# Kernel tuning notes

Hardware: AMD Instinct MI355X
Metric: run time of the kernel (lower is better)

The kernel has to match this reference:

```python
import jax, jax.numpy as jnp
import numpy as np

B, T, C = 2, 2048, 2048
H, HD = 16, 128          # n_head, head_dim
LORA = C // 4            # kv_lora_rank = n_embd // compression_ratio
RD = HD // 2             # qk_rope_dim
ND = HD - RD             # qk_nope_dim
THETA = 100000.0


def setup_inputs() -> dict:
    key = jax.random.key(0)
    k0, k1, k2, k3, k4 = jax.random.split(key, 5)
    s = 0.02
    return {
        "x": jax.random.normal(k0, (B, T, C), dtype=jnp.float32),
        "Wq": jax.random.normal(k1, (C, H * HD), dtype=jnp.float32) * s,
        "Wkva": jax.random.normal(k2, (C, LORA + RD), dtype=jnp.float32) * s,
        "Wkvb": jax.random.normal(k3, (LORA, H * ND), dtype=jnp.float32) * s,
        "Wo": jax.random.normal(k4, (H * HD, C), dtype=jnp.float32) * s,
    }


def apply_rope(x, theta=THETA):
    # x: [B, H, T, D] with D even; interleaved complex rotation (torch.view_as_complex style)
    b, h, t, d = x.shape
    freqs = 1.0 / (theta ** (jnp.arange(0, d, 2, dtype=jnp.float32) / d))  # [D/2]
    ang = jnp.arange(t, dtype=jnp.float32)[:, None] * freqs[None, :]       # [T, D/2]
    cos, sin = jnp.cos(ang), jnp.sin(ang)
    xr = x.reshape(b, h, t, d // 2, 2)
    x0, x1 = xr[..., 0], xr[..., 1]
    o0 = x0 * cos - x1 * sin
    o1 = x0 * sin + x1 * cos
    return jnp.stack([o0, o1], axis=-1).reshape(b, h, t, d)


def reference(x, Wq, Wkva, Wkvb, Wo):
    Bx, Tx, Cx = x.shape
    # query projection -> [B, H, T, HD]
    q = (x @ Wq).reshape(Bx, Tx, H, HD).transpose(0, 2, 1, 3)
    # compressed KV + shared (MQA) rope key
    ckv = x @ Wkva                                  # [B, T, LORA+RD]
    kv_latent = ckv[..., :LORA]                     # [B, T, LORA]
    k_rope = ckv[..., LORA:]                        # [B, T, RD]
    # decompress nope part of K (== nope part of V)
    kv = (kv_latent @ Wkvb).reshape(Bx, Tx, H, ND).transpose(0, 2, 1, 3)  # [B,H,T,ND]
    k_rope = jnp.broadcast_to(k_rope[:, None, :, :], (Bx, H, Tx, RD))
    q_nope, q_rope = q[..., :ND], q[..., ND:]
    q_rope = apply_rope(q_rope)
    k_rope = apply_rope(k_rope)
    qf = jnp.concatenate([q_nope, q_rope], axis=-1)               # [B,H,T,HD]
    kf = jnp.concatenate([kv, k_rope], axis=-1)                   # [B,H,T,HD]
    vf = jnp.concatenate([kv, jnp.zeros_like(k_rope)], axis=-1)   # [B,H,T,HD]
    scale = 1.0 / np.sqrt(HD).astype(np.float32)
    att = jnp.einsum("bhtd,bhsd->bhts", qf, kf) * scale           # [B,H,T,T]
    causal = jnp.tril(jnp.ones((Tx, Tx), dtype=bool))
    att = jnp.where(causal, att, -jnp.inf)
    att = jax.nn.softmax(att, axis=-1)
    y = jnp.einsum("bhts,bhsd->bhtd", att, vf)                    # [B,H,T,HD]
    y = y.transpose(0, 2, 1, 3).reshape(Bx, Tx, H * HD)
    return y @ Wo
```

## Files before the change

kernel.cpp:

```cpp
#include <hip/hip_runtime.h>
#include <hip/hip_bf16.h>
#include <math.h>

#define B_ 2
#define T_ 2048
#define C_ 2048
#define H_ 16
#define HD_ 128
#define LORA_ 512
#define RD_ 64
#define ND_ 64
#define BT_ (B_*T_)
#define NKVA_ 576
#define NKVAP_ 640
#define LOG2_THETA 16.609640474436812f

typedef __bf16 bf16x8 __attribute__((ext_vector_type(8)));
typedef float  f32x4  __attribute__((ext_vector_type(4)));

#define MFMA16(a,b,c) __builtin_amdgcn_mfma_f32_16x16x32_bf16((a),(b),(c),0,0,0)

__device__ static inline void load_lds16(const __bf16* g, __bf16* l) {
  auto* lp = (__attribute__((address_space(3))) char*)(uintptr_t)(l);
  auto* gp = (const __attribute__((address_space(1))) char*)(g);
  __builtin_amdgcn_global_load_lds(gp, lp, 16, 0, 0);
}

__device__ static inline unsigned pkbf(float a, float b) {
  union { __bf16 h[2]; unsigned u; } v;
  v.h[0] = (__bf16)a; v.h[1] = (__bf16)b;
  return v.u;
}

__global__ __launch_bounds__(256) void k_cast_x(const float* __restrict__ x,
                                                __bf16* __restrict__ xb, int n) {
  int idx = blockIdx.x * 256 + threadIdx.x;
  if (idx < n) xb[idx] = (__bf16)x[idx];
}

__global__ __launch_bounds__(256) void k_tcast(const float* __restrict__ src,
                                               __bf16* __restrict__ dst,
                                               int K, int N, int NP) {
  __shared__ float tile[32][33];
  int k0 = blockIdx.x * 32;
  int n0 = blockIdx.y * 32;
  int tx = threadIdx.x & 31, ty = threadIdx.x >> 5;
  for (int i = ty; i < 32; i += 8) {
    int n = n0 + tx;
    tile[i][tx] = (n < N) ? src[(size_t)(k0 + i) * N + n] : 0.0f;
  }
  __syncthreads();
  for (int i = ty; i < 32; i += 8) {
    dst[(size_t)(n0 + i) * K + k0 + tx] = (__bf16)tile[tx][i];
  }
}

__global__ __launch_bounds__(256) void k_tcast_wo(const float* __restrict__ Wo,
                                                  __bf16* __restrict__ dst) {
  __shared__ float tile[32][33];
  int kc0 = blockIdx.x * 32;
  int n0  = blockIdx.y * 32;
  int rbase = (kc0 >> 6) * 128 + (kc0 & 63);
  int tx = threadIdx.x & 31, ty = threadIdx.x >> 5;
  for (int i = ty; i < 32; i += 8)
    tile[i][tx] = Wo[(size_t)(rbase + i) * C_ + n0 + tx];
  __syncthreads();
  for (int i = ty; i < 32; i += 8)
    dst[(size_t)(n0 + i) * 1024 + kc0 + tx] = (__bf16)tile[tx][i];
}

__global__ __launch_bounds__(256) void k_gemm_bt(const __bf16* __restrict__ A,
                                                 const __bf16* __restrict__ B,
                                                 float* __restrict__ C,
                                                 int M, int N, int K) {
  __shared__ __align__(16) __bf16 As[2][128 * 32];
  __shared__ __align__(16) __bf16 Bs[2][128 * 32];
  const int tid  = threadIdx.x;
  const int lane = tid & 63;
  const int wave = tid >> 6;
  const int bm = blockIdx.x, bn = blockIdx.y;
  const int r0 = tid >> 2;
  const int c8 = (tid & 3) * 8;
  const __bf16* Ag = A + (size_t)(bm * 128 + r0) * K + c8;
  const __bf16* Bg = B + (size_t)(bn * 128 + r0) * K + c8;
  const int wr = (wave >> 1) * 64, wc = (wave & 1) * 64;
  const int fr = lane & 15, fk = (lane >> 4) * 8;
  const f32x4 fzero = {0.f, 0.f, 0.f, 0.f};
  f32x4 acc[4][4];
#pragma unroll
  for (int i = 0; i < 4; ++i)
#pragma unroll
    for (int j = 0; j < 4; ++j) acc[i][j] = fzero;

  load_lds16(Ag,                  &As[0][tid * 8]);
  load_lds16(Ag + (size_t)64 * K, &As[0][tid * 8 + 2048]);
  load_lds16(Bg,                  &Bs[0][tid * 8]);
  load_lds16(Bg + (size_t)64 * K, &Bs[0][tid * 8 + 2048]);

  int buf = 0;
  for (int k0 = 0; k0 < K; k0 += 32) {
    __syncthreads();
    if (k0 + 32 < K) {
      const int nb = buf ^ 1;
      load_lds16(Ag + k0 + 32,                  &As[nb][tid * 8]);
      load_lds16(Ag + (size_t)64 * K + k0 + 32, &As[nb][tid * 8 + 2048]);
      load_lds16(Bg + k0 + 32,                  &Bs[nb][tid * 8]);
      load_lds16(Bg + (size_t)64 * K + k0 + 32, &Bs[nb][tid * 8 + 2048]);
    }
    bf16x8 af[4], bfg[4];
#pragma unroll
    for (int i = 0; i < 4; ++i) af[i]  = *(const bf16x8*)&As[buf][(wr + i * 16 + fr) * 32 + fk];
#pragma unroll
    for (int j = 0; j < 4; ++j) bfg[j] = *(const bf16x8*)&Bs[buf][(wc + j * 16 + fr) * 32 + fk];
#pragma unroll
    for (int i = 0; i < 4; ++i)
#pragma unroll
      for (int j = 0; j < 4; ++j)
        acc[i][j] = MFMA16(af[i], bfg[j], acc[i][j]);
    buf ^= 1;
  }
  const int rbase = (lane >> 4) * 4;
  float* Cb = C + (size_t)(bm * 128 + wr + rbase) * N + bn * 128 + wc + fr;
#pragma unroll
  for (int i = 0; i < 4; ++i)
#pragma unroll
    for (int j = 0; j < 4; ++j)
#pragma unroll
      for (int r = 0; r < 4; ++r)
        Cb[(size_t)(i * 16 + r) * N + j * 16] = acc[i][j][r];
}

__global__ __launch_bounds__(256) void k_rope_q(const float* __restrict__ q,
                                                __bf16* __restrict__ qf) {
  const float scale2 = 1.4426950408889634f / 11.313708498984760f;
  int idx = blockIdx.x * 256 + threadIdx.x;
  int d  = idx & 127;
  int t  = (idx >> 7) & 2047;
  int bh = idx >> 18;
  int h  = bh & 15, b = bh >> 4;
  const float* qrow = q + ((size_t)(b * T_ + t)) * 2048 + h * 128;
  float v;
  if (d < 64) {
    v = qrow[d];
  } else {
    int i = (d - 64) >> 1;
    float freq = exp2f(-((float)(2 * i) / 64.0f) * LOG2_THETA);
    float ang = (float)t * freq;
    float c = cosf(ang), s = sinf(ang);
    float x0 = qrow[64 + 2 * i], x1 = qrow[64 + 2 * i + 1];
    v = (d & 1) ? (x0 * s + x1 * c) : (x0 * c - x1 * s);
  }
  qf[idx] = (__bf16)(v * scale2);
}


__global__ __launch_bounds__(256) void k_rope_kf(const float* __restrict__ ckv,
                                                 __bf16* __restrict__ Kp) {
  int idx = blockIdx.x * 256 + threadIdx.x;
  int i = idx & 31;
  int t = (idx >> 5) & 2047;
  int h = (idx >> 16) & 15;
  int b = idx >> 20;
  const float* src = ckv + ((size_t)(b * T_ + t)) * NKVAP_ + 512;
  float freq = exp2f(-((float)(2 * i) / 64.0f) * LOG2_THETA);
  float ang = (float)t * freq;
  float c = cosf(ang), s = sinf(ang);
  float x0 = src[2 * i], x1 = src[2 * i + 1];
  float v0 = x0 * c - x1 * s;
  float v1 = x0 * s + x1 * c;
  int bh = b * 16 + h;
  int tile = t >> 6, cg = (t >> 4) & 3, frk = t & 15;
  int kg = 2 + (i >> 4), qd = (i >> 2) & 3, e = (2 * i) & 7;
  size_t off = (((size_t)(bh * 32 + tile) * 16) + cg * 4 + kg) * 512
             + (qd * 16 + frk) * 8 + e;
  *(unsigned*)(Kp + off) = pkbf(v0, v1);
}

__global__ __launch_bounds__(256) void k_cast_kvl(const float* __restrict__ ckv,
                                                  __bf16* __restrict__ kvl) {
  int idx = blockIdx.x * 256 + threadIdx.x;
  int r = idx >> 9, c = idx & 511;
  kvl[idx] = (__bf16)ckv[(size_t)r * NKVAP_ + c];
}

__global__ __launch_bounds__(256) void k_pack_kv(const float* __restrict__ kv,
                                                 __bf16* __restrict__ Kp,
                                                 __bf16* __restrict__ Vp) {
  __shared__ float tile[64][65];
  const int bh = blockIdx.x;
  const int b = bh >> 4, h = bh & 15;
  const int t0 = blockIdx.y * 64;
  const int tilei = t0 >> 6;
  const int tid = threadIdx.x;
  const int i0 = tid >> 4, d4 = (tid & 15) * 4;
  const int kg = d4 >> 5, qd = (d4 >> 3) & 3, e = d4 & 7;
#pragma unroll
  for (int p = 0; p < 4; ++p) {
    int i = i0 + p * 16;
    const float* src = kv + ((size_t)(b * T_ + t0 + i)) * 1024 + h * 64 + d4;
    float4 v = *(const float4*)src;
    tile[i][d4] = v.x; tile[i][d4 + 1] = v.y; tile[i][d4 + 2] = v.z; tile[i][d4 + 3] = v.w;
    union { __bf16 hh[4]; uint2 u; } o;
    o.hh[0] = (__bf16)v.x; o.hh[1] = (__bf16)v.y; o.hh[2] = (__bf16)v.z; o.hh[3] = (__bf16)v.w;
    const int cg = i >> 4, frk = i & 15;
    size_t koff = (((size_t)(bh * 32 + tilei) * 16) + cg * 4 + kg) * 512
                + (qd * 16 + frk) * 8 + e;
    *(uint2*)(Kp + koff) = o.u;
  }
  __syncthreads();
  const int dd = tid >> 2, tc0 = (tid & 3) * 16;
  __bf16 outv[16];
#pragma unroll
  for (int j = 0; j < 16; ++j) outv[j] = (__bf16)tile[tc0 + j][dd];
  const int g = dd >> 4, frv = dd & 15;
  const int ks = tc0 >> 5, qv = (tc0 >> 3) & 3;
  size_t voff = (((size_t)(bh * 32 + tilei) * 8) + g * 2 + ks) * 512
              + (qv * 16 + frv) * 8;
  *(bf16x8*)(Vp + voff) = *(bf16x8*)&outv[0];
  *(bf16x8*)(Vp + voff + 128) = *(bf16x8*)&outv[8];
}

__global__ __launch_bounds__(512, 4) void k_attn(const __bf16* __restrict__ qf,
                                                 const __bf16* __restrict__ Kp,
                                                 const __bf16* __restrict__ Vp,
                                                 __bf16* __restrict__ yc) {
  const int blk = blockIdx.x;
  const int bh = blk & 31;
  const int qt = 31 - (blk >> 5);
  const int b = bh >> 4, h = bh & 15;
  const int qbase = qt * 64;
  const int tid = threadIdx.x;
  const int lane = tid & 63, wave = tid >> 6;
  const int w4 = wave & 3, par = wave >> 2;
  const int fr = lane & 15, quad = lane >> 4, fk8 = quad * 8;

  __shared__ __align__(16) f32x4 mrgO[4][64][4];
  __shared__ float mrgML[4][64][2];

  const int qi = qbase + w4 * 16 + fr;
  const __bf16* qb = qf + ((size_t)bh * T_ + qi) * HD_;
  bf16x8 aq[4];
#pragma unroll
  for (int g = 0; g < 4; ++g) aq[g] = *(const bf16x8*)(qb + g * 32 + fk8);

  const f32x4 fzero = {0.f, 0.f, 0.f, 0.f};
  f32x4 accO[4];
#pragma unroll
  for (int g = 0; g < 4; ++g) accO[g] = fzero;
  float m = -1e30f, l = 0.f;

  const __bf16* kb = Kp + (size_t)bh * 32 * 8192 + (size_t)lane * 8;
  const __bf16* vb = Vp + (size_t)bh * 32 * 4096 + (size_t)lane * 8;
  const int srcA = (quad & 1) * 32 + fr, srcB = srcA + 16;
  const int hi = quad >> 1;

  for (int s0 = par * 64; s0 <= qbase; s0 += 128) {
    const __bf16* kt = kb + (size_t)(s0 >> 6) * 8192;
    const __bf16* vt = vb + (size_t)(s0 >> 6) * 4096;

    bf16x8 kr[4][4];
#pragma unroll
    for (int cg = 0; cg < 4; ++cg)
#pragma unroll
      for (int kg = 0; kg < 4; ++kg)
        kr[cg][kg] = *(const bf16x8*)(kt + (cg * 4 + kg) * 512);

    f32x4 accST[4];
#pragma unroll
    for (int cg = 0; cg < 4; ++cg) accST[cg] = fzero;
    __builtin_amdgcn_s_setprio(1);
#pragma unroll
    for (int cg = 0; cg < 4; ++cg) {
#pragma unroll
      for (int kg = 0; kg < 4; ++kg)
        accST[cg] = MFMA16(kr[cg][kg], aq[kg], accST[cg]);
    }
    __builtin_amdgcn_s_setprio(0);

    bf16x8 vr[4][2];
#pragma unroll
    for (int g = 0; g < 4; ++g)
#pragma unroll
      for (int ks = 0; ks < 2; ++ks)
        vr[g][ks] = *(const bf16x8*)(vt + (g * 2 + ks) * 512);

    float lmax = -1e30f;
    if (s0 == qbase) {
#pragma unroll
      for (int cg = 0; cg < 4; ++cg) {
#pragma unroll
        for (int r = 0; r < 4; ++r) {
          const int key = s0 + cg * 16 + quad * 4 + r;
          float v = accST[cg][r];
          v = (key <= qi) ? v : -1e30f;
          accST[cg][r] = v;
          lmax = fmaxf(lmax, v);
        }
      }
    } else {
#pragma unroll
      for (int cg = 0; cg < 4; ++cg) {
#pragma unroll
        for (int r = 0; r < 4; ++r) lmax = fmaxf(lmax, accST[cg][r]);
      }
    }
    lmax = fmaxf(lmax, __shfl_xor(lmax, 16, 64));
    lmax = fmaxf(lmax, __shfl_xor(lmax, 32, 64));

    if (!__all(lmax <= m + 8.0f)) {
      const float mn = fmaxf(m, lmax);
      const float alpha = exp2f(m - mn);
      l *= alpha;
#pragma unroll
      for (int g = 0; g < 4; ++g)
#pragma unroll
        for (int r = 0; r < 4; ++r) accO[g][r] *= alpha;
      m = mn;
    }

    float lsum = 0.f;
    unsigned pk0[4], pk1[4];
#pragma unroll
    for (int cg = 0; cg < 4; ++cg) {
      float p0 = exp2f(accST[cg][0] - m);
      float p1 = exp2f(accST[cg][1] - m);
      float p2 = exp2f(accST[cg][2] - m);
      float p3 = exp2f(accST[cg][3] - m);
      lsum += (p0 + p1) + (p2 + p3);
      pk0[cg] = pkbf(p0, p1);
      pk1[cg] = pkbf(p2, p3);
    }
    lsum += __shfl_xor(lsum, 16, 64);
    lsum += __shfl_xor(lsum, 32, 64);
    l += lsum;

#pragma unroll
    for (int ks = 0; ks < 2; ++ks) {
      int a0 = __shfl((int)pk0[2 * ks], srcA, 64);
      int b0 = __shfl((int)pk0[2 * ks + 1], srcA, 64);
      int a1 = __shfl((int)pk1[2 * ks], srcA, 64);
      int b1 = __shfl((int)pk1[2 * ks + 1], srcA, 64);
      int a2 = __shfl((int)pk0[2 * ks], srcB, 64);
      int b2 = __shfl((int)pk0[2 * ks + 1], srcB, 64);
      int a3 = __shfl((int)pk1[2 * ks], srcB, 64);
      int b3 = __shfl((int)pk1[2 * ks + 1], srcB, 64);
      union { int i[4]; bf16x8 v; } pf;
      pf.i[0] = hi ? b0 : a0;
      pf.i[1] = hi ? b1 : a1;
      pf.i[2] = hi ? b2 : a2;
      pf.i[3] = hi ? b3 : a3;
      __builtin_amdgcn_s_setprio(1);
#pragma unroll
      for (int g = 0; g < 4; ++g)
        accO[g] = MFMA16(vr[g][ks], pf.v, accO[g]);
      __builtin_amdgcn_s_setprio(0);
    }
  }

  if (par) {
#pragma unroll
    for (int g = 0; g < 4; ++g) mrgO[w4][lane][g] = accO[g];
    mrgML[w4][lane][0] = m;
    mrgML[w4][lane][1] = l;
  }
  __syncthreads();
  if (!par) {
    const float m1 = mrgML[w4][lane][0];
    const float l1 = mrgML[w4][lane][1];
    const float mn = fmaxf(m, m1);
    const float a0 = exp2f(m - mn), a1 = exp2f(m1 - mn);
    const float lt = l * a0 + l1 * a1;
    const float linv = 1.0f / lt;
    __bf16* yb = yc + ((size_t)(b * T_ + qi)) * 1024 + h * 64 + quad * 4;
#pragma unroll
    for (int g = 0; g < 4; ++g) {
      f32x4 o1 = mrgO[w4][lane][g];
      union { unsigned u[2]; uint2 v; } o;
      o.u[0] = pkbf((accO[g][0] * a0 + o1[0] * a1) * linv,
                    (accO[g][1] * a0 + o1[1] * a1) * linv);
      o.u[1] = pkbf((accO[g][2] * a0 + o1[2] * a1) * linv,
                    (accO[g][3] * a0 + o1[3] * a1) * linv);
      *(uint2*)(yb + g * 16) = o.v;
    }
  }
}

extern "C" void kernel_launch(void* const* d_in, const int* in_sizes, int n_in,
                              void* d_out, int out_size, void* d_ws, size_t ws_size,
                              hipStream_t stream) {
  const float* x    = (const float*)d_in[0];
  const float* Wq   = (const float*)d_in[1];
  const float* Wkva = (const float*)d_in[2];
  const float* Wkvb = (const float*)d_in[3];
  const float* Wo   = (const float*)d_in[4];
  float* out = (float*)d_out;
  char* ws = (char*)d_ws;

  size_t off = 0;
  __bf16* xb    = (__bf16*)(ws + off); off += (size_t)BT_ * C_ * 2;
  __bf16* WqT   = (__bf16*)(ws + off); off += (size_t)2048 * 2048 * 2;
  __bf16* WkvaT = (__bf16*)(ws + off); off += (size_t)NKVAP_ * 2048 * 2;
  __bf16* WkvbT = (__bf16*)(ws + off); off += (size_t)1024 * 512 * 2;
  __bf16* WoTc  = (__bf16*)(ws + off); off += (size_t)2048 * 1024 * 2;
  float*  q     = (float*)(ws + off);  off += (size_t)BT_ * 2048 * 4;
  float*  ckv   = (float*)(ws + off);  off += (size_t)BT_ * NKVAP_ * 4;
  __bf16* kvl   = (__bf16*)(ws + off); off += (size_t)BT_ * 512 * 2;
  float*  kv    = (float*)(ws + off);  off += (size_t)BT_ * 1024 * 4;
  __bf16* qfb   = (__bf16*)(ws + off); off += (size_t)B_ * H_ * T_ * HD_ * 2;
  __bf16* yc    = (__bf16*)(ws + off); off += (size_t)BT_ * 1024 * 2;
  __bf16* Kp = (__bf16*)q;
  __bf16* Vp = (__bf16*)((char*)q + (size_t)B_ * H_ * T_ * HD_ * 2);

  k_cast_x<<<(BT_ * C_) / 256, 256, 0, stream>>>(x, xb, BT_ * C_);
  k_tcast<<<dim3(2048 / 32, 2048 / 32), 256, 0, stream>>>(Wq, WqT, 2048, 2048, 2048);
  k_tcast<<<dim3(2048 / 32, NKVAP_ / 32), 256, 0, stream>>>(Wkva, WkvaT, 2048, NKVA_, NKVAP_);
  k_tcast<<<dim3(512 / 32, 1024 / 32), 256, 0, stream>>>(Wkvb, WkvbT, 512, 1024, 1024);
  k_tcast_wo<<<dim3(1024 / 32, 2048 / 32), 256, 0, stream>>>(Wo, WoTc);

  k_gemm_bt<<<dim3(BT_ / 128, 2048 / 128), 256, 0, stream>>>(xb, WqT, q, BT_, 2048, 2048);
  k_gemm_bt<<<dim3(BT_ / 128, NKVAP_ / 128), 256, 0, stream>>>(xb, WkvaT, ckv, BT_, NKVAP_, 2048);

  k_rope_q<<<(B_ * H_ * T_ * HD_) / 256, 256, 0, stream>>>(q, qfb);
  k_cast_kvl<<<(BT_ * 512) / 256, 256, 0, stream>>>(ckv, kvl);

  k_gemm_bt<<<dim3(BT_ / 128, 1024 / 128), 256, 0, stream>>>(kvl, WkvbT, kv, BT_, 1024, 512);
  k_pack_kv<<<dim3(B_ * H_, T_ / 64), 256, 0, stream>>>(kv, Kp, Vp);
  k_rope_kf<<<(B_ * H_ * T_ * 32) / 256, 256, 0, stream>>>(ckv, Kp);

  k_attn<<<(T_ / 64) * B_ * H_, 512, 0, stream>>>(qfb, Kp, Vp, yc);

  k_gemm_bt<<<dim3(BT_ / 128, 2048 / 128), 256, 0, stream>>>(yc, WoTc, out, BT_, 2048, 1024);
}
```

Measured before the change: 336.1 us.

## Fuse Q and KV-A projections into one GEMM with rope and cast epilogues

The separate Q and compressed-KV GEMMs become a single launch over a combined weight matrix of 2688 rows, assuming WkvaT sits directly after WqT in the workspace. The epilogue applies scaling and RoPE and writes bf16 q straight into the attention layout. It writes the latent part of KV as bf16 and keeps only the rope columns of ckv in fp32. This removes the fp32 q round trip through memory plus the standalone rope_q and cast_kvl kernels. The cost is a heavier epilogue with per-element cos/sin evaluation and lane shuffles.

```diff
diff --git a/kernel.cpp b/kernel.cpp
--- a/kernel.cpp
+++ b/kernel.cpp
@@ -130,27 +130,121 @@
         Cb[(size_t)(i * 16 + r) * N + j * 16] = acc[i][j][r];
 }
 
-__global__ __launch_bounds__(256) void k_rope_q(const float* __restrict__ q,
-                                                __bf16* __restrict__ qf) {
+__global__ __launch_bounds__(256) void k_gemm_qkva(const __bf16* __restrict__ A,
+                                                   const __bf16* __restrict__ Bq,
+                                                   __bf16* __restrict__ qf,
+                                                   __bf16* __restrict__ kvl,
+                                                   float* __restrict__ ckv) {
+  const int K = 2048;
+  __shared__ __align__(16) __bf16 As[2][128 * 32];
+  __shared__ __align__(16) __bf16 Bs[2][128 * 32];
+  const int tid  = threadIdx.x;
+  const int lane = tid & 63;
+  const int wave = tid >> 6;
+  const int bm = blockIdx.x, bn = blockIdx.y;
+  const int r0 = tid >> 2;
+  const int c8 = (tid & 3) * 8;
+  const __bf16* Ag = A  + (size_t)(bm * 128 + r0) * K + c8;
+  const __bf16* Bg = Bq + (size_t)(bn * 128 + r0) * K + c8;
+  const int wr = (wave >> 1) * 64, wc = (wave & 1) * 64;
+  const int fr = lane & 15, fk = (lane >> 4) * 8;
+  const f32x4 fzero = {0.f, 0.f, 0.f, 0.f};
+  f32x4 acc[4][4];
+#pragma unroll
+  for (int i = 0; i < 4; ++i)
+#pragma unroll
+    for (int j = 0; j < 4; ++j) acc[i][j] = fzero;
+
+  load_lds16(Ag,                  &As[0][tid * 8]);
+  load_lds16(Ag + (size_t)64 * K, &As[0][tid * 8 + 2048]);
+  load_lds16(Bg,                  &Bs[0][tid * 8]);
+  load_lds16(Bg + (size_t)64 * K, &Bs[0][tid * 8 + 2048]);
+
+  int buf = 0;
+  for (int k0 = 0; k0 < K; k0 += 32) {
+    __syncthreads();
+    if (k0 + 32 < K) {
+      const int nb = buf ^ 1;
+      load_lds16(Ag + k0 + 32,                  &As[nb][tid * 8]);
+      load_lds16(Ag + (size_t)64 * K + k0 + 32, &As[nb][tid * 8 + 2048]);
+      load_lds16(Bg + k0 + 32,                  &Bs[nb][tid * 8]);
+      load_lds16(Bg + (size_t)64 * K + k0 + 32, &Bs[nb][tid * 8 + 2048]);
+    }
+    bf16x8 af[4], bfg[4];
+#pragma unroll
+    for (int i = 0; i < 4; ++i) af[i]  = *(const bf16x8*)&As[buf][(wr + i * 16 + fr) * 32 + fk];
+#pragma unroll
+    for (int j = 0; j < 4; ++j) bfg[j] = *(const bf16x8*)&Bs[buf][(wc + j * 16 + fr) * 32 + fk];
+#pragma unroll
+    for (int i = 0; i < 4; ++i)
+#pragma unroll
+      for (int j = 0; j < 4; ++j)
+        acc[i][j] = MFMA16(af[i], bfg[j], acc[i][j]);
+    buf ^= 1;
+  }
+
+  const int rbase = (lane >> 4) * 4;
   const float scale2 = 1.4426950408889634f / 11.313708498984760f;
-  int idx = blockIdx.x * 256 + threadIdx.x;
-  int d  = idx & 127;
-  int t  = (idx >> 7) & 2047;
-  int bh = idx >> 18;
-  int h  = bh & 15, b = bh >> 4;
-  const float* qrow = q + ((size_t)(b * T_ + t)) * 2048 + h * 128;
-  float v;
-  if (d < 64) {
-    v = qrow[d];
+
+  if (bn < 16) {
+    const int h = bn;
+#pragma unroll
+    for (int i = 0; i < 4; ++i) {
+#pragma unroll
+      for (int j = 0; j < 4; ++j) {
+        const int d = wc + j * 16 + fr;
+#pragma unroll
+        for (int r = 0; r < 4; ++r) {
+          const int tg = bm * 128 + wr + rbase + i * 16 + r;
+          const int b = tg >> 11, tin = tg & 2047;
+          float v = acc[i][j][r];
+          float vo = __shfl_xor(v, 1);
+          float o;
+          if (d < 64) {
+            o = v * scale2;
+          } else {
+            const int ip = (d - 64) >> 1;
+            float freq = exp2f(-((float)(2 * ip) / 64.0f) * LOG2_THETA);
+            float ang = (float)tin * freq;
+            float c = cosf(ang), s = sinf(ang);
+            o = ((fr & 1) == 0) ? (v * c - vo * s) : (vo * s + v * c);
+            o *= scale2;
+          }
+          float op = __shfl_xor(o, 1);
+          if ((fr & 1) == 0) {
+            *(unsigned*)(qf + (((size_t)(b * 16 + h) * 2048 + tin) * 128 + d)) =
+                pkbf(o, op);
+          }
+        }
+      }
+    }
+  } else if (bn < 20) {
+    const int cb = (bn - 16) * 128;
+#pragma unroll
+    for (int i = 0; i < 4; ++i) {
+#pragma unroll
+      for (int j = 0; j < 4; ++j) {
+        const int c = cb + wc + j * 16 + fr;
+#pragma unroll
+        for (int r = 0; r < 4; ++r) {
+          const int tg = bm * 128 + wr + rbase + i * 16 + r;
+          float v = acc[i][j][r];
+          float vo = __shfl_xor(v, 1);
+          if ((fr & 1) == 0)
+            *(unsigned*)(kvl + ((size_t)tg * 512 + c)) = pkbf(v, vo);
+        }
+      }
+    }
   } else {
-    int i = (d - 64) >> 1;
-    float freq = exp2f(-((float)(2 * i) / 64.0f) * LOG2_THETA);
-    float ang = (float)t * freq;
-    float c = cosf(ang), s = sinf(ang);
-    float x0 = qrow[64 + 2 * i], x1 = qrow[64 + 2 * i + 1];
-    v = (d & 1) ? (x0 * s + x1 * c) : (x0 * c - x1 * s);
-  }
-  qf[idx] = (__bf16)(v * scale2);
+    float* Cb = ckv + (size_t)(bm * 128 + wr + rbase) * NKVAP_ + 512 + wc + fr;
+#pragma unroll
+    for (int i = 0; i < 4; ++i)
+#pragma unroll
+      for (int j = 0; j < 4; ++j)
+#pragma unroll
+        for (int r = 0; r < 4; ++r)
+          Cb[(size_t)(i * 16 + r) * NKVAP_ + j * 16] = acc[i][j][r];
+  }
 }
 
 
@@ -176,13 +270,6 @@
   *(unsigned*)(Kp + off) = pkbf(v0, v1);
 }
 
-__global__ __launch_bounds__(256) void k_cast_kvl(const float* __restrict__ ckv,
-                                                  __bf16* __restrict__ kvl) {
-  int idx = blockIdx.x * 256 + threadIdx.x;
-  int r = idx >> 9, c = idx & 511;
-  kvl[idx] = (__bf16)ckv[(size_t)r * NKVAP_ + c];
-}
-
 __global__ __launch_bounds__(256) void k_pack_kv(const float* __restrict__ kv,
                                                  __bf16* __restrict__ Kp,
                                                  __bf16* __restrict__ Vp) {
@@ -417,11 +504,7 @@
   k_tcast<<<dim3(512 / 32, 1024 / 32), 256, 0, stream>>>(Wkvb, WkvbT, 512, 1024, 1024);
   k_tcast_wo<<<dim3(1024 / 32, 2048 / 32), 256, 0, stream>>>(Wo, WoTc);
 
-  k_gemm_bt<<<dim3(BT_ / 128, 2048 / 128), 256, 0, stream>>>(xb, WqT, q, BT_, 2048, 2048);
-  k_gemm_bt<<<dim3(BT_ / 128, NKVAP_ / 128), 256, 0, stream>>>(xb, WkvaT, ckv, BT_, NKVAP_, 2048);
-
-  k_rope_q<<<(B_ * H_ * T_ * HD_) / 256, 256, 0, stream>>>(q, qfb);
-  k_cast_kvl<<<(BT_ * 512) / 256, 256, 0, stream>>>(ckv, kvl);
+  k_gemm_qkva<<<dim3(BT_ / 128, 2688 / 128), 256, 0, stream>>>(xb, WqT, qfb, kvl, ckv);
 
   k_gemm_bt<<<dim3(BT_ / 128, 1024 / 128), 256, 0, stream>>>(kvl, WkvbT, kv, BT_, 1024, 512);
   k_pack_kv<<<dim3(B_ * H_, T_ / 64), 256, 0, stream>>>(kv, Kp, Vp);
```

Result: slower. 348.7 us (+3.7%).

## Split GEMM K dimension across two intra-block warp groups with LDS reduction

Applied to the files above, without the earlier changes.

Each GEMM block now runs 512 threads as two 256-thread halves. Each half accumulates the same 128x128 output tile over half of the K range, using its own double-buffered LDS region. At the end, one half writes its partial sums to LDS and the other adds them and stores to global memory. This doubles the waves per tile to hide latency, at the cost of 64KB LDS per block, an extra reduction pass and more register pressure under launch_bounds(512,4).

```diff
diff --git a/kernel.cpp b/kernel.cpp
--- a/kernel.cpp
+++ b/kernel.cpp
@@ -69,21 +69,25 @@
     dst[(size_t)(n0 + i) * 1024 + kc0 + tx] = (__bf16)tile[tx][i];
 }
 
-__global__ __launch_bounds__(256) void k_gemm_bt(const __bf16* __restrict__ A,
-                                                 const __bf16* __restrict__ B,
-                                                 float* __restrict__ C,
-                                                 int M, int N, int K) {
-  __shared__ __align__(16) __bf16 As[2][128 * 32];
-  __shared__ __align__(16) __bf16 Bs[2][128 * 32];
+__global__ __launch_bounds__(512, 4) void k_gemm_bt(const __bf16* __restrict__ A,
+                                                    const __bf16* __restrict__ B,
+                                                    float* __restrict__ C,
+                                                    int M, int N, int K) {
+  __shared__ __align__(16) char smem[65536];
   const int tid  = threadIdx.x;
+  const int half = tid >> 8;
+  const int tid_h = tid & 255;
   const int lane = tid & 63;
-  const int wave = tid >> 6;
+  const int wave4 = (tid >> 6) & 3;
   const int bm = blockIdx.x, bn = blockIdx.y;
-  const int r0 = tid >> 2;
-  const int c8 = (tid & 3) * 8;
-  const __bf16* Ag = A + (size_t)(bm * 128 + r0) * K + c8;
-  const __bf16* Bg = B + (size_t)(bn * 128 + r0) * K + c8;
-  const int wr = (wave >> 1) * 64, wc = (wave & 1) * 64;
+  const int Kh = K >> 1, kbase = half * Kh;
+  __bf16* As = (__bf16*)smem + (size_t)half * 16384;
+  __bf16* Bs = As + 8192;
+  const int r0 = tid_h >> 2;
+  const int c8 = (tid_h & 3) * 8;
+  const __bf16* Ag = A + (size_t)(bm * 128 + r0) * K + kbase + c8;
+  const __bf16* Bg = B + (size_t)(bn * 128 + r0) * K + kbase + c8;
+  const int wr = (wave4 >> 1) * 64, wc = (wave4 & 1) * 64;
   const int fr = lane & 15, fk = (lane >> 4) * 8;
   const f32x4 fzero = {0.f, 0.f, 0.f, 0.f};
   f32x4 acc[4][4];
@@ -92,26 +96,28 @@
 #pragma unroll
     for (int j = 0; j < 4; ++j) acc[i][j] = fzero;
 
-  load_lds16(Ag,                  &As[0][tid * 8]);
-  load_lds16(Ag + (size_t)64 * K, &As[0][tid * 8 + 2048]);
-  load_lds16(Bg,                  &Bs[0][tid * 8]);
-  load_lds16(Bg + (size_t)64 * K, &Bs[0][tid * 8 + 2048]);
+  load_lds16(Ag,                  &As[tid_h * 8]);
+  load_lds16(Ag + (size_t)64 * K, &As[tid_h * 8 + 2048]);
+  load_lds16(Bg,                  &Bs[tid_h * 8]);
+  load_lds16(Bg + (size_t)64 * K, &Bs[tid_h * 8 + 2048]);
 
   int buf = 0;
-  for (int k0 = 0; k0 < K; k0 += 32) {
+  for (int k0 = 0; k0 < Kh; k0 += 32) {
     __syncthreads();
-    if (k0 + 32 < K) {
+    if (k0 + 32 < Kh) {
       const int nb = buf ^ 1;
-      load_lds16(Ag + k0 + 32,                  &As[nb][tid * 8]);
-      load_lds16(Ag + (size_t)64 * K + k0 + 32, &As[nb][tid * 8 + 2048]);
-      load_lds16(Bg + k0 + 32,                  &Bs[nb][tid * 8]);
-      load_lds16(Bg + (size_t)64 * K + k0 + 32, &Bs[nb][tid * 8 + 2048]);
+      load_lds16(Ag + k0 + 32,                  &As[nb * 4096 + tid_h * 8]);
+      load_lds16(Ag + (size_t)64 * K + k0 + 32, &As[nb * 4096 + tid_h * 8 + 2048]);
+      load_lds16(Bg + k0 + 32,                  &Bs[nb * 4096 + tid_h * 8]);
+      load_lds16(Bg + (size_t)64 * K + k0 + 32, &Bs[nb * 4096 + tid_h * 8 + 2048]);
     }
     bf16x8 af[4], bfg[4];
 #pragma unroll
-    for (int i = 0; i < 4; ++i) af[i]  = *(const bf16x8*)&As[buf][(wr + i * 16 + fr) * 32 + fk];
-#pragma unroll
-    for (int j = 0; j < 4; ++j) bfg[j] = *(const bf16x8*)&Bs[buf][(wc + j * 16 + fr) * 32 + fk];
+    for (int i = 0; i < 4; ++i)
+      af[i]  = *(const bf16x8*)&As[buf * 4096 + (wr + i * 16 + fr) * 32 + fk];
+#pragma unroll
+    for (int j = 0; j < 4; ++j)
+      bfg[j] = *(const bf16x8*)&Bs[buf * 4096 + (wc + j * 16 + fr) * 32 + fk];
 #pragma unroll
     for (int i = 0; i < 4; ++i)
 #pragma unroll
@@ -119,15 +125,31 @@
         acc[i][j] = MFMA16(af[i], bfg[j], acc[i][j]);
     buf ^= 1;
   }
+
+  __syncthreads();
+  float* mrg = (float*)smem;
   const int rbase = (lane >> 4) * 4;
-  float* Cb = C + (size_t)(bm * 128 + wr + rbase) * N + bn * 128 + wc + fr;
-#pragma unroll
-  for (int i = 0; i < 4; ++i)
-#pragma unroll
-    for (int j = 0; j < 4; ++j)
-#pragma unroll
-      for (int r = 0; r < 4; ++r)
-        Cb[(size_t)(i * 16 + r) * N + j * 16] = acc[i][j][r];
+  if (half) {
+#pragma unroll
+    for (int i = 0; i < 4; ++i)
+#pragma unroll
+      for (int j = 0; j < 4; ++j)
+#pragma unroll
+        for (int r = 0; r < 4; ++r)
+          mrg[(wr + i * 16 + rbase + r) * 128 + wc + j * 16 + fr] = acc[i][j][r];
+  }
+  __syncthreads();
+  if (!half) {
+    float* Cb = C + (size_t)(bm * 128 + wr + rbase) * N + bn * 128 + wc + fr;
+#pragma unroll
+    for (int i = 0; i < 4; ++i)
+#pragma unroll
+      for (int j = 0; j < 4; ++j)
+#pragma unroll
+        for (int r = 0; r < 4; ++r)
+          Cb[(size_t)(i * 16 + r) * N + j * 16] =
+              acc[i][j][r] + mrg[(wr + i * 16 + rbase + r) * 128 + wc + j * 16 + fr];
+  }
 }
 
 __global__ __launch_bounds__(256) void k_rope_q(const float* __restrict__ q,
@@ -417,17 +439,17 @@
   k_tcast<<<dim3(512 / 32, 1024 / 32), 256, 0, stream>>>(Wkvb, WkvbT, 512, 1024, 1024);
   k_tcast_wo<<<dim3(1024 / 32, 2048 / 32), 256, 0, stream>>>(Wo, WoTc);
 
-  k_gemm_bt<<<dim3(BT_ / 128, 2048 / 128), 256, 0, stream>>>(xb, WqT, q, BT_, 2048, 2048);
-  k_gemm_bt<<<dim3(BT_ / 128, NKVAP_ / 128), 256, 0, stream>>>(xb, WkvaT, ckv, BT_, NKVAP_, 2048);
+  k_gemm_bt<<<dim3(BT_ / 128, 2048 / 128), 512, 0, stream>>>(xb, WqT, q, BT_, 2048, 2048);
+  k_gemm_bt<<<dim3(BT_ / 128, NKVAP_ / 128), 512, 0, stream>>>(xb, WkvaT, ckv, BT_, NKVAP_, 2048);
 
   k_rope_q<<<(B_ * H_ * T_ * HD_) / 256, 256, 0, stream>>>(q, qfb);
   k_cast_kvl<<<(BT_ * 512) / 256, 256, 0, stream>>>(ckv, kvl);
 
-  k_gemm_bt<<<dim3(BT_ / 128, 1024 / 128), 256, 0, stream>>>(kvl, WkvbT, kv, BT_, 1024, 512);
+  k_gemm_bt<<<dim3(BT_ / 128, 1024 / 128), 512, 0, stream>>>(kvl, WkvbT, kv, BT_, 1024, 512);
   k_pack_kv<<<dim3(B_ * H_, T_ / 64), 256, 0, stream>>>(kv, Kp, Vp);
   k_rope_kf<<<(B_ * H_ * T_ * 32) / 256, 256, 0, stream>>>(ckv, Kp);
 
   k_attn<<<(T_ / 64) * B_ * H_, 512, 0, stream>>>(qfb, Kp, Vp, yc);
 
-  k_gemm_bt<<<dim3(BT_ / 128, 2048 / 128), 256, 0, stream>>>(yc, WoTc, out, BT_, 2048, 1024);
-}
+  k_gemm_bt<<<dim3(BT_ / 128, 2048 / 128), 512, 0, stream>>>(yc, WoTc, out, BT_, 2048, 1024);
+}
```

New measurement: 335.9 us. About the same (-0.1%).

## Pair causal query tiles per attention block and fuse Q/KV-A projection GEMMs

Applied to the files above, without the earlier changes.

Each attention block now handles two query tiles, p and 31-p, one after the other. Every block therefore does about the same amount of causal work, and the grid shrinks by half. Separately, the Q and compressed-KV projections now run as one GEMM launch. It reads WqT and WkvaT as one contiguous weight matrix and sends each column-block's output to the q or ckv buffer. This removes one launch and the tail imbalance of the triangular attention, but each attention block now runs two serial phases with an extra barrier, and the fused GEMM depends on the two weight buffers sitting next to each other in the workspace.

```diff
diff --git a/kernel.cpp b/kernel.cpp
--- a/kernel.cpp
+++ b/kernel.cpp
@@ -128,6 +128,71 @@
 #pragma unroll
       for (int r = 0; r < 4; ++r)
         Cb[(size_t)(i * 16 + r) * N + j * 16] = acc[i][j][r];
+}
+
+__global__ __launch_bounds__(256) void k_gemm_qkva(const __bf16* __restrict__ A,
+                                                   const __bf16* __restrict__ Bq,
+                                                   float* __restrict__ q,
+                                                   float* __restrict__ ckv) {
+  const int K = 2048;
+  __shared__ __align__(16) __bf16 As[2][128 * 32];
+  __shared__ __align__(16) __bf16 Bs[2][128 * 32];
+  const int tid  = threadIdx.x;
+  const int lane = tid & 63;
+  const int wave = tid >> 6;
+  const int bm = blockIdx.x, bn = blockIdx.y;
+  const int r0 = tid >> 2;
+  const int c8 = (tid & 3) * 8;
+  const __bf16* Ag = A  + (size_t)(bm * 128 + r0) * K + c8;
+  const __bf16* Bg = Bq + (size_t)(bn * 128 + r0) * K + c8;
+  const int wr = (wave >> 1) * 64, wc = (wave & 1) * 64;
+  const int fr = lane & 15, fk = (lane >> 4) * 8;
+  const f32x4 fzero = {0.f, 0.f, 0.f, 0.f};
+  f32x4 acc[4][4];
+#pragma unroll
+  for (int i = 0; i < 4; ++i)
+#pragma unroll
+    for (int j = 0; j < 4; ++j) acc[i][j] = fzero;
+
+  load_lds16(Ag,                  &As[0][tid * 8]);
+  load_lds16(Ag + (size_t)64 * K, &As[0][tid * 8 + 2048]);
+  load_lds16(Bg,                  &Bs[0][tid * 8]);
+  load_lds16(Bg + (size_t)64 * K, &Bs[0][tid * 8 + 2048]);
+
+  int buf = 0;
+  for (int k0 = 0; k0 < K; k0 += 32) {
+    __syncthreads();
+    if (k0 + 32 < K) {
+      const int nb = buf ^ 1;
+      load_lds16(Ag + k0 + 32,                  &As[nb][tid * 8]);
+      load_lds16(Ag + (size_t)64 * K + k0 + 32, &As[nb][tid * 8 + 2048]);
+      load_lds16(Bg + k0 + 32,                  &Bs[nb][tid * 8]);
+      load_lds16(Bg + (size_t)64 * K + k0 + 32, &Bs[nb][tid * 8 + 2048]);
+    }
+    bf16x8 af[4], bfg[4];
+#pragma unroll
+    for (int i = 0; i < 4; ++i) af[i]  = *(const bf16x8*)&As[buf][(wr + i * 16 + fr) * 32 + fk];
+#pragma unroll
+    for (int j = 0; j < 4; ++j) bfg[j] = *(const bf16x8*)&Bs[buf][(wc + j * 16 + fr) * 32 + fk];
+#pragma unroll
+    for (int i = 0; i < 4; ++i)
+#pragma unroll
+      for (int j = 0; j < 4; ++j)
+        acc[i][j] = MFMA16(af[i], bfg[j], acc[i][j]);
+    buf ^= 1;
+  }
+  const int rbase = (lane >> 4) * 4;
+  float* Cb;
+  int stride;
+  if (bn < 16) { Cb = q   + (size_t)(bm * 128 + wr + rbase) * 2048 + bn * 128 + wc + fr;        stride = 2048; }
+  else         { Cb = ckv + (size_t)(bm * 128 + wr + rbase) * NKVAP_ + (bn - 16) * 128 + wc + fr; stride = NKVAP_; }
+#pragma unroll
+  for (int i = 0; i < 4; ++i)
+#pragma unroll
+    for (int j = 0; j < 4; ++j)
+#pragma unroll
+      for (int r = 0; r < 4; ++r)
+        Cb[(size_t)(i * 16 + r) * stride + j * 16] = acc[i][j][r];
 }
 
 __global__ __launch_bounds__(256) void k_rope_q(const float* __restrict__ q,
@@ -226,9 +291,8 @@
                                                  __bf16* __restrict__ yc) {
   const int blk = blockIdx.x;
   const int bh = blk & 31;
-  const int qt = 31 - (blk >> 5);
+  const int p  = blk >> 5;
   const int b = bh >> 4, h = bh & 15;
-  const int qbase = qt * 64;
   const int tid = threadIdx.x;
   const int lane = tid & 63, wave = tid >> 6;
   const int w4 = wave & 3, par = wave >> 2;
@@ -237,152 +301,159 @@
   __shared__ __align__(16) f32x4 mrgO[4][64][4];
   __shared__ float mrgML[4][64][2];
 
-  const int qi = qbase + w4 * 16 + fr;
-  const __bf16* qb = qf + ((size_t)bh * T_ + qi) * HD_;
-  bf16x8 aq[4];
-#pragma unroll
-  for (int g = 0; g < 4; ++g) aq[g] = *(const bf16x8*)(qb + g * 32 + fk8);
-
-  const f32x4 fzero = {0.f, 0.f, 0.f, 0.f};
-  f32x4 accO[4];
-#pragma unroll
-  for (int g = 0; g < 4; ++g) accO[g] = fzero;
-  float m = -1e30f, l = 0.f;
-
   const __bf16* kb = Kp + (size_t)bh * 32 * 8192 + (size_t)lane * 8;
   const __bf16* vb = Vp + (size_t)bh * 32 * 4096 + (size_t)lane * 8;
   const int srcA = (quad & 1) * 32 + fr, srcB = srcA + 16;
   const int hi = quad >> 1;
-
-  for (int s0 = par * 64; s0 <= qbase; s0 += 128) {
-    const __bf16* kt = kb + (size_t)(s0 >> 6) * 8192;
-    const __bf16* vt = vb + (size_t)(s0 >> 6) * 4096;
-
-    bf16x8 kr[4][4];
-#pragma unroll
-    for (int cg = 0; cg < 4; ++cg)
-#pragma unroll
-      for (int kg = 0; kg < 4; ++kg)
-        kr[cg][kg] = *(const bf16x8*)(kt + (cg * 4 + kg) * 512);
-
-    f32x4 accST[4];
-#pragma unroll
-    for (int cg = 0; cg < 4; ++cg) accST[cg] = fzero;
-    __builtin_amdgcn_s_setprio(1);
-#pragma unroll
-    for (int cg = 0; cg < 4; ++cg) {
-#pragma unroll
-      for (int kg = 0; kg < 4; ++kg)
-        accST[cg] = MFMA16(kr[cg][kg], aq[kg], accST[cg]);
-    }
-    __builtin_amdgcn_s_setprio(0);
-
-    bf16x8 vr[4][2];
-#pragma unroll
-    for (int g = 0; g < 4; ++g)
-#pragma unroll
-      for (int ks = 0; ks < 2; ++ks)
-        vr[g][ks] = *(const bf16x8*)(vt + (g * 2 + ks) * 512);
-
-    float lmax = -1e30f;
-    if (s0 == qbase) {
+  const f32x4 fzero = {0.f, 0.f, 0.f, 0.f};
+
+  auto process = [&](int qt) {
+    const int qbase = qt * 64;
+    const int qi = qbase + w4 * 16 + fr;
+    const __bf16* qb = qf + ((size_t)bh * T_ + qi) * HD_;
+    bf16x8 aq[4];
+#pragma unroll
+    for (int g = 0; g < 4; ++g) aq[g] = *(const bf16x8*)(qb + g * 32 + fk8);
+
+    f32x4 accO[4];
+#pragma unroll
+    for (int g = 0; g < 4; ++g) accO[g] = fzero;
+    float m = -1e30f, l = 0.f;
+
+    for (int s0 = par * 64; s0 <= qbase; s0 += 128) {
+      const __bf16* kt = kb + (size_t)(s0 >> 6) * 8192;
+      const __bf16* vt = vb + (size_t)(s0 >> 6) * 4096;
+
+      bf16x8 kr[4][4];
+#pragma unroll
+      for (int cg = 0; cg < 4; ++cg)
+#pragma unroll
+        for (int kg = 0; kg < 4; ++kg)
+          kr[cg][kg] = *(const bf16x8*)(kt + (cg * 4 + kg) * 512);
+
+      f32x4 accST[4];
+#pragma unroll
+      for (int cg = 0; cg < 4; ++cg) accST[cg] = fzero;
+      __builtin_amdgcn_s_setprio(1);
 #pragma unroll
       for (int cg = 0; cg < 4; ++cg) {
 #pragma unroll
-        for (int r = 0; r < 4; ++r) {
-          const int key = s0 + cg * 16 + quad * 4 + r;
-          float v = accST[cg][r];
-          v = (key <= qi) ? v : -1e30f;
-          accST[cg][r] = v;
-          lmax = fmaxf(lmax, v);
+        for (int kg = 0; kg < 4; ++kg)
+          accST[cg] = MFMA16(kr[cg][kg], aq[kg], accST[cg]);
+      }
+      __builtin_amdgcn_s_setprio(0);
+
+      bf16x8 vr[4][2];
+#pragma unroll
+      for (int g = 0; g < 4; ++g)
+#pragma unroll
+        for (int ks = 0; ks < 2; ++ks)
+          vr[g][ks] = *(const bf16x8*)(vt + (g * 2 + ks) * 512);
+
+      float lmax = -1e30f;
+      if (s0 == qbase) {
+#pragma unroll
+        for (int cg = 0; cg < 4; ++cg) {
+#pragma unroll
+          for (int r = 0; r < 4; ++r) {
+            const int key = s0 + cg * 16 + quad * 4 + r;
+            float v = accST[cg][r];
+            v = (key <= qi) ? v : -1e30f;
+            accST[cg][r] = v;
+            lmax = fmaxf(lmax, v);
+          }
+        }
+      } else {
+#pragma unroll
+        for (int cg = 0; cg < 4; ++cg) {
+#pragma unroll
+          for (int r = 0; r < 4; ++r) lmax = fmaxf(lmax, accST[cg][r]);
         }
       }
-    } else {
+      lmax = fmaxf(lmax, __shfl_xor(lmax, 16, 64));
+      lmax = fmaxf(lmax, __shfl_xor(lmax, 32, 64));
+
+      if (!__all(lmax <= m + 8.0f)) {
+        const float mn = fmaxf(m, lmax);
+        const float alpha = exp2f(m - mn);
+        l *= alpha;
+#pragma unroll
+        for (int g = 0; g < 4; ++g)
+#pragma unroll
+          for (int r = 0; r < 4; ++r) accO[g][r] *= alpha;
+        m = mn;
+      }
+
+      float lsum = 0.f;
+      unsigned pk0[4], pk1[4];
 #pragma unroll
       for (int cg = 0; cg < 4; ++cg) {
-#pragma unroll
-        for (int r = 0; r < 4; ++r) lmax = fmaxf(lmax, accST[cg][r]);
+        float p0 = exp2f(accST[cg][0] - m);
+        float p1 = exp2f(accST[cg][1] - m);
+        float p2 = exp2f(accST[cg][2] - m);
+        float p3 = exp2f(accST[cg][3] - m);
+        lsum += (p0 + p1) + (p2 + p3);
+        pk0[cg] = pkbf(p0, p1);
+        pk1[cg] = pkbf(p2, p3);
+      }
+      lsum += __shfl_xor(lsum, 16, 64);
+      lsum += __shfl_xor(lsum, 32, 64);
+      l += lsum;
+
+#pragma unroll
+      for (int ks = 0; ks < 2; ++ks) {
+        int a0 = __shfl((int)pk0[2 * ks], srcA, 64);
+        int b0 = __shfl((int)pk0[2 * ks + 1], srcA, 64);
+        int a1 = __shfl((int)pk1[2 * ks], srcA, 64);
+        int b1 = __shfl((int)pk1[2 * ks + 1], srcA, 64);
+        int a2 = __shfl((int)pk0[2 * ks], srcB, 64);
+        int b2 = __shfl((int)pk0[2 * ks + 1], srcB, 64);
+        int a3 = __shfl((int)pk1[2 * ks], srcB, 64);
+        int b3 = __shfl((int)pk1[2 * ks + 1], srcB, 64);
+        union { int i[4]; bf16x8 v; } pf;
+        pf.i[0] = hi ? b0 : a0;
+        pf.i[1] = hi ? b1 : a1;
+        pf.i[2] = hi ? b2 : a2;
+        pf.i[3] = hi ? b3 : a3;
+        __builtin_amdgcn_s_setprio(1);
+#pragma unroll
+        for (int g = 0; g < 4; ++g)
+          accO[g] = MFMA16(vr[g][ks], pf.v, accO[g]);
+        __builtin_amdgcn_s_setprio(0);
       }
     }
-    lmax = fmaxf(lmax, __shfl_xor(lmax, 16, 64));
-    lmax = fmaxf(lmax, __shfl_xor(lmax, 32, 64));
-
-    if (!__all(lmax <= m + 8.0f)) {
-      const float mn = fmaxf(m, lmax);
-      const float alpha = exp2f(m - mn);
-      l *= alpha;
-#pragma unroll
-      for (int g = 0; g < 4; ++g)
-#pragma unroll
-        for (int r = 0; r < 4; ++r) accO[g][r] *= alpha;
-      m = mn;
+
+    if (par) {
+#pragma unroll
+      for (int g = 0; g < 4; ++g) mrgO[w4][lane][g] = accO[g];
+      mrgML[w4][lane][0] = m;
+      mrgML[w4][lane][1] = l;
     }
-
-    float lsum = 0.f;
-    unsigned pk0[4], pk1[4];
-#pragma unroll
-    for (int cg = 0; cg < 4; ++cg) {
-      float p0 = exp2f(accST[cg][0] - m);
-      float p1 = exp2f(accST[cg][1] - m);
-      float p2 = exp2f(accST[cg][2] - m);
-      float p3 = exp2f(accST[cg][3] - m);
-      lsum += (p0 + p1) + (p2 + p3);
-      pk0[cg] = pkbf(p0, p1);
-      pk1[cg] = pkbf(p2, p3);
+    __syncthreads();
+    if (!par) {
+      const float m1 = mrgML[w4][lane][0];
+      const float l1 = mrgML[w4][lane][1];
+      const float mn = fmaxf(m, m1);
+      const float a0 = exp2f(m - mn), a1 = exp2f(m1 - mn);
+      const float lt = l * a0 + l1 * a1;
+      const float linv = 1.0f / lt;
+      __bf16* yb = yc + ((size_t)(b * T_ + qi)) * 1024 + h * 64 + quad * 4;
+#pragma unroll
+      for (int g = 0; g < 4; ++g) {
+        f32x4 o1 = mrgO[w4][lane][g];
+        union { unsigned u[2]; uint2 v; } o;
+        o.u[0] = pkbf((accO[g][0] * a0 + o1[0] * a1) * linv,
+                      (accO[g][1] * a0 + o1[1] * a1) * linv);
+        o.u[1] = pkbf((accO[g][2] * a0 + o1[2] * a1) * linv,
+                      (accO[g][3] * a0 + o1[3] * a1) * linv);
+        *(uint2*)(yb + g * 16) = o.v;
+      }
     }
-    lsum += __shfl_xor(lsum, 16, 64);
-    lsum += __shfl_xor(lsum, 32, 64);
-    l += lsum;
-
-#pragma unroll
-    for (int ks = 0; ks < 2; ++ks) {
-      int a0 = __shfl((int)pk0[2 * ks], srcA, 64);
-      int b0 = __shfl((int)pk0[2 * ks + 1], srcA, 64);
-      int a1 = __shfl((int)pk1[2 * ks], srcA, 64);
-      int b1 = __shfl((int)pk1[2 * ks + 1], srcA, 64);
-      int a2 = __shfl((int)pk0[2 * ks], srcB, 64);
-      int b2 = __shfl((int)pk0[2 * ks + 1], srcB, 64);
-      int a3 = __shfl((int)pk1[2 * ks], srcB, 64);
-      int b3 = __shfl((int)pk1[2 * ks + 1], srcB, 64);
-      union { int i[4]; bf16x8 v; } pf;
-      pf.i[0] = hi ? b0 : a0;
-      pf.i[1] = hi ? b1 : a1;
-      pf.i[2] = hi ? b2 : a2;
-      pf.i[3] = hi ? b3 : a3;
-      __builtin_amdgcn_s_setprio(1);
-#pragma unroll
-      for (int g = 0; g < 4; ++g)
-        accO[g] = MFMA16(vr[g][ks], pf.v, accO[g]);
-      __builtin_amdgcn_s_setprio(0);
-    }
-  }
-
-  if (par) {
-#pragma unroll
-    for (int g = 0; g < 4; ++g) mrgO[w4][lane][g] = accO[g];
-    mrgML[w4][lane][0] = m;
-    mrgML[w4][lane][1] = l;
-  }
+  };
+
+  process(p);
   __syncthreads();
-  if (!par) {
-    const float m1 = mrgML[w4][lane][0];
-    const float l1 = mrgML[w4][lane][1];
-    const float mn = fmaxf(m, m1);
-    const float a0 = exp2f(m - mn), a1 = exp2f(m1 - mn);
-    const float lt = l * a0 + l1 * a1;
-    const float linv = 1.0f / lt;
-    __bf16* yb = yc + ((size_t)(b * T_ + qi)) * 1024 + h * 64 + quad * 4;
-#pragma unroll
-    for (int g = 0; g < 4; ++g) {
-      f32x4 o1 = mrgO[w4][lane][g];
-      union { unsigned u[2]; uint2 v; } o;
-      o.u[0] = pkbf((accO[g][0] * a0 + o1[0] * a1) * linv,
-                    (accO[g][1] * a0 + o1[1] * a1) * linv);
-      o.u[1] = pkbf((accO[g][2] * a0 + o1[2] * a1) * linv,
-                    (accO[g][3] * a0 + o1[3] * a1) * linv);
-      *(uint2*)(yb + g * 16) = o.v;
-    }
-  }
+  process(31 - p);
 }
 
 extern "C" void kernel_launch(void* const* d_in, const int* in_sizes, int n_in,
@@ -417,8 +488,7 @@
   k_tcast<<<dim3(512 / 32, 1024 / 32), 256, 0, stream>>>(Wkvb, WkvbT, 512, 1024, 1024);
   k_tcast_wo<<<dim3(1024 / 32, 2048 / 32), 256, 0, stream>>>(Wo, WoTc);
 
-  k_gemm_bt<<<dim3(BT_ / 128, 2048 / 128), 256, 0, stream>>>(xb, WqT, q, BT_, 2048, 2048);
-  k_gemm_bt<<<dim3(BT_ / 128, NKVAP_ / 128), 256, 0, stream>>>(xb, WkvaT, ckv, BT_, NKVAP_, 2048);
+  k_gemm_qkva<<<dim3(BT_ / 128, 2688 / 128), 256, 0, stream>>>(xb, WqT, q, ckv);
 
   k_rope_q<<<(B_ * H_ * T_ * HD_) / 256, 256, 0, stream>>>(q, qfb);
   k_cast_kvl<<<(BT_ * 512) / 256, 256, 0, stream>>>(ckv, kvl);
@@ -427,7 +497,7 @@
   k_pack_kv<<<dim3(B_ * H_, T_ / 64), 256, 0, stream>>>(kv, Kp, Vp);
   k_rope_kf<<<(B_ * H_ * T_ * 32) / 256, 256, 0, stream>>>(ckv, Kp);
 
-  k_attn<<<(T_ / 64) * B_ * H_, 512, 0, stream>>>(qfb, Kp, Vp, yc);
+  k_attn<<<(T_ / 128) * B_ * H_, 512, 0, stream>>>(qfb, Kp, Vp, yc);
 
   k_gemm_bt<<<dim3(BT_ / 128, 2048 / 128), 256, 0, stream>>>(yc, WoTc, out, BT_, 2048, 1024);
 }
```

New measurement: 323.7 us. 3.7% less time.
